# Optimization experiments

Measured on AMD Instinct MI355X. Metric: run time of the kernel, lower is better.

The kernel has to match this reference:

```python
import jax, jax.numpy as jnp
import numpy as np

DIM = 192
HEADS = 4
EPS_LN = 1e-5
EPS_NORM = 1e-12


def _layernorm(x, w, b):
    # x: [b, c, h, w]; normalize over channel dim (equiv to 'b (h w) c' LN over last axis)
    mu = jnp.mean(x, axis=1, keepdims=True)
    var = jnp.mean((x - mu) ** 2, axis=1, keepdims=True)
    return (x - mu) / jnp.sqrt(var + EPS_LN) * w[None, :, None, None] + b[None, :, None, None]


def _conv1x1(x, w):
    # w: [out_c, in_c]
    return jnp.einsum('bchw,oc->bohw', x, w)


def _dwconv3x3(x, w):
    # w: [c, 1, 3, 3], depthwise (groups = c), padding 1
    return jax.lax.conv_general_dilated(
        x, w, window_strides=(1, 1), padding='SAME',
        feature_group_count=x.shape[1],
        dimension_numbers=('NCHW', 'OIHW', 'NCHW'))


def _l2norm(x):
    # F.normalize(dim=-1): x / max(||x||_2, eps)
    n = jnp.sqrt(jnp.sum(x * x, axis=-1, keepdims=True))
    return x / jnp.maximum(n, EPS_NORM)


def setup_inputs() -> dict:
    key = jax.random.key(0)
    ks = jax.random.split(key, 10)
    b, c, h, w = 8, DIM, 128, 128
    inp = {
        'xx': jax.random.normal(ks[0], (b, c, h, w), jnp.float32),
        'q_in': jax.random.normal(ks[1], (b, c, h, w), jnp.float32),
        'ln_w': jnp.ones((c,), jnp.float32),
        'ln_b': jnp.zeros((c,), jnp.float32),
        'w_q': jax.random.normal(ks[2], (c, c), jnp.float32) * 0.02,
        'w_k': jax.random.normal(ks[3], (c, c), jnp.float32) * 0.02,
        'w_v': jax.random.normal(ks[4], (c, c), jnp.float32) * 0.02,
        'wd_q': jax.random.normal(ks[5], (c, 1, 3, 3), jnp.float32) * 0.1,
        'wd_k': jax.random.normal(ks[6], (c, 1, 3, 3), jnp.float32) * 0.1,
        'wd_v': jax.random.normal(ks[7], (c, 1, 3, 3), jnp.float32) * 0.1,
        'w_proj': jax.random.normal(ks[8], (c, c), jnp.float32) * 0.02,
        'temperature': jnp.ones((HEADS, 1, 1), jnp.float32),
    }
    return inp


def reference(xx, q_in, ln_w, ln_b, w_q, w_k, w_v, wd_q, wd_k, wd_v, w_proj, temperature):
    b, c, h, w = xx.shape
    hw = h * w
    dh = c // HEADS  # per-head channel dim

    x_n = _layernorm(xx, ln_w, ln_b)
    q_n = _layernorm(q_in, ln_w, ln_b)

    q = _dwconv3x3(_conv1x1(q_n, w_q), wd_q)
    k = _dwconv3x3(_conv1x1(x_n, w_k), wd_k)
    v = _dwconv3x3(_conv1x1(x_n, w_v), wd_v)

    # b (head c) h w -> b head c (h w)
    q = q.reshape(b, HEADS, dh, hw)
    k = k.reshape(b, HEADS, dh, hw)
    v = v.reshape(b, HEADS, dh, hw)

    q = _l2norm(q)
    k = _l2norm(k)

    # channel-channel attention: [b, head, dh, dh]
    attn = jnp.einsum('bhcn,bhdn->bhcd', q, k) * temperature[None]
    attn = jax.nn.softmax(attn, axis=-1)

    out = jnp.einsum('bhcd,bhdn->bhcn', attn, v)  # [b, head, dh, hw]
    out = out.reshape(b, c, h, w)
    out = _conv1x1(out, w_proj) + q_in
    return out
```

## Files before the change

kernel.cpp:

```cpp
#include <hip/hip_runtime.h>
#include <hip/hip_bf16.h>
#include <stdint.h>

#define HWSZ 16384
#define CCH 192
#define NB 8
#define NHEAD 4
#define DHEAD 48

typedef unsigned short u16;
typedef __bf16 bf16x8 __attribute__((ext_vector_type(8)));
typedef float f32x4 __attribute__((ext_vector_type(4)));
typedef short s16x8 __attribute__((ext_vector_type(8)));
typedef short s16x4 __attribute__((ext_vector_type(4)));

__device__ __forceinline__ float b2f(u16 h){
  union { unsigned u; float f; } v; v.u = ((unsigned)h) << 16; return v.f;
}
__device__ __forceinline__ u16 f2b(float f){
  union { float f; unsigned u; } v; v.f = f;
  unsigned r = v.u + 0x7fffu + ((v.u >> 16) & 1u);
  return (u16)(r >> 16);
}

__global__ __launch_bounds__(256) void k_wpack(
    const float* __restrict__ wq, const float* __restrict__ wk,
    const float* __restrict__ wv, u16* __restrict__ o)
{
  int m = blockIdx.x;
  const float* src = (m == 0) ? wq : (m == 1) ? wk : wv;
  u16* dst = o + (size_t)m * CCH * CCH;
  int tid = threadIdx.x;
  #pragma unroll
  for (int i = 0; i < 36; ++i){
    int e = (i * 256 + tid) * 4;
    float4 v = *(const float4*)(src + e);
    s16x4 pk;
    pk[0] = (short)f2b(v.x); pk[1] = (short)f2b(v.y);
    pk[2] = (short)f2b(v.z); pk[3] = (short)f2b(v.w);
    *(s16x4*)(dst + e) = pk;
  }
}

template<int NG>
__global__ __launch_bounds__(256) void k_lngemm(
    const float* __restrict__ x, const float* __restrict__ lnw,
    const float* __restrict__ lnb,
    const u16* __restrict__ W0, const u16* __restrict__ W1,
    u16* __restrict__ O0, u16* __restrict__ O1)
{
  __shared__ u16 lnT[12672];
  __shared__ float red[2048];
  __shared__ float mures[128];
  __shared__ float lwlb[384];
  int tid = threadIdx.x;
  int b   = blockIdx.y;
  int p0  = blockIdx.x * 64;
  int cq  = tid >> 4;
  int q   = tid & 15;

  float wl = 0.f, bl = 0.f;
  if (tid >= 64){
    int c = tid - 64;
    wl = lnw[c]; bl = lnb[c];
  }

  float4 v[12];
  {
    const float* xb = x + (size_t)b * CCH * HWSZ + p0;
    #pragma unroll
    for (int i = 0; i < 12; ++i)
      v[i] = *(const float4*)(xb + (size_t)(i * 16 + cq) * HWSZ + q * 4);
  }
  {
    float4 ps  = make_float4(0.f, 0.f, 0.f, 0.f);
    float4 pss = make_float4(0.f, 0.f, 0.f, 0.f);
    #pragma unroll
    for (int i = 0; i < 12; ++i){
      ps.x += v[i].x; ps.y += v[i].y; ps.z += v[i].z; ps.w += v[i].w;
      pss.x += v[i].x * v[i].x; pss.y += v[i].y * v[i].y;
      pss.z += v[i].z * v[i].z; pss.w += v[i].w * v[i].w;
    }
    *(float4*)(&red[cq * 64 + q * 4])        = ps;
    *(float4*)(&red[1024 + cq * 64 + q * 4]) = pss;
  }
  __syncthreads();

  if (tid < 64){
    float s = 0.f, ss2 = 0.f;
    #pragma unroll
    for (int j = 0; j < 16; ++j){
      s   += red[j * 64 + tid];
      ss2 += red[1024 + j * 64 + tid];
    }
    float mu  = s * (1.f / CCH);
    float var = ss2 * (1.f / CCH) - mu * mu;
    mures[tid]      = mu;
    mures[64 + tid] = rsqrtf(var + 1e-5f);
  } else {
    int c = tid - 64;
    lwlb[c] = wl; lwlb[192 + c] = bl;
  }
  __syncthreads();

  {
    float m0 = mures[q * 4 + 0], m1 = mures[q * 4 + 1];
    float m2 = mures[q * 4 + 2], m3 = mures[q * 4 + 3];
    float r0 = mures[64 + q * 4 + 0], r1 = mures[64 + q * 4 + 1];
    float r2 = mures[64 + q * 4 + 2], r3 = mures[64 + q * 4 + 3];
    #pragma unroll
    for (int i = 0; i < 12; ++i){
      int c = i * 16 + cq;
      float lw_ = lwlb[c], lb_ = lwlb[192 + c];
      s16x4 pk;
      pk[0] = (short)f2b((v[i].x - m0) * r0 * lw_ + lb_);
      pk[1] = (short)f2b((v[i].y - m1) * r1 * lw_ + lb_);
      pk[2] = (short)f2b((v[i].z - m2) * r2 * lw_ + lb_);
      pk[3] = (short)f2b((v[i].w - m3) * r3 * lw_ + lb_);
      int kb   = c >> 5, kr = c & 31;
      int tile = (kr >> 2) & 1;
      int mr   = ((kr >> 3) << 2) | (kr & 3);
      int ti   = (kb * 4 + (q >> 2)) * 2 + tile;
      *(s16x4*)(&lnT[ti * 264 + mr * 16 + (q & 3) * 4]) = pk;
    }
  }
  __syncthreads();

  int lane = tid & 63, wid = tid >> 6;
  int quad = lane >> 4, r = lane & 15;
  int wm = wid * 48;
  const u16* A0 = W0 + (size_t)wm * CCH;
  const u16* A1 = (NG == 2) ? (W1 + (size_t)wm * CCH) : nullptr;
  f32x4 acc0[3][4] = {};
  f32x4 acc1[3][4] = {};
  unsigned lvb = (unsigned)(uintptr_t)(&lnT[0]) + 2u * (unsigned)(r + quad * 64);
  #pragma unroll
  for (int kb = 0; kb < 6; ++kb){
    int k0 = kb * 32;
    bf16x8 a0[3], a1[3];
    #pragma unroll
    for (int i = 0; i < 3; ++i)
      a0[i] = *(const bf16x8*)(A0 + (size_t)(i * 16 + r) * CCH + k0 + quad * 8);
    if (NG == 2){
      #pragma unroll
      for (int i = 0; i < 3; ++i)
        a1[i] = *(const bf16x8*)(A1 + (size_t)(i * 16 + r) * CCH + k0 + quad * 8);
    }
    s16x4 lo[4], hi[4];
    #pragma unroll
    for (int j = 0; j < 4; ++j){
      unsigned a = lvb + (unsigned)kb * 4224u + (unsigned)j * 1056u;
      asm volatile("ds_read_b64_tr_b16 %0, %1" : "=&v"(lo[j]) : "v"(a));
      asm volatile("ds_read_b64_tr_b16 %0, %1 offset:528" : "=&v"(hi[j]) : "v"(a));
    }
    asm volatile("s_waitcnt lgkmcnt(0)" ::: "memory");
    __builtin_amdgcn_sched_barrier(0);
    #pragma unroll
    for (int j = 0; j < 4; ++j){
      union { s16x8 s; bf16x8 b; } u;
      u.s = __builtin_shufflevector(lo[j], hi[j], 0, 1, 2, 3, 4, 5, 6, 7);
      #pragma unroll
      for (int i = 0; i < 3; ++i)
        acc0[i][j] = __builtin_amdgcn_mfma_f32_16x16x32_bf16(a0[i], u.b, acc0[i][j], 0, 0, 0);
      if (NG == 2){
        #pragma unroll
        for (int i = 0; i < 3; ++i)
          acc1[i][j] = __builtin_amdgcn_mfma_f32_16x16x32_bf16(a1[i], u.b, acc1[i][j], 0, 0, 0);
      }
    }
  }
  size_t ob = (size_t)b * CCH * HWSZ;
  #pragma unroll
  for (int i = 0; i < 3; ++i){
    #pragma unroll
    for (int rg = 0; rg < 4; ++rg){
      int o = wm + i * 16 + quad * 4 + rg;
      size_t rowb = ob + (size_t)o * HWSZ;
      #pragma unroll
      for (int j = 0; j < 4; ++j){
        int n = p0 + j * 16 + r;
        O0[rowb + n] = f2b(acc0[i][j][rg]);
        if (NG == 2) O1[rowb + n] = f2b(acc1[i][j][rg]);
      }
    }
  }
}

__global__ __launch_bounds__(256) void k_dw3(
    const float* __restrict__ wq, const float* __restrict__ wk,
    const float* __restrict__ wv,
    u16* __restrict__ bq, u16* __restrict__ bk, u16* __restrict__ bv,
    float* __restrict__ ssq_q, float* __restrict__ ssq_k)
{
  int tid = threadIdx.x;
  int bc  = blockIdx.x;
  int z   = blockIdx.y;
  int c   = bc % CCH;
  const float* wd = (z == 0) ? wq : (z == 1) ? wk : wv;
  u16* buf = (z == 0) ? bq : (z == 1) ? bk : bv;
  float w[9];
  #pragma unroll
  for (int t = 0; t < 9; ++t) w[t] = wd[c * 9 + t];
  u16* p = buf + (size_t)bc * HWSZ;

  int xseg = tid & 15, ygrp = tid >> 4;
  int x0 = xseg * 8, y0 = ygrp * 8;

  s16x8 zz = {0,0,0,0,0,0,0,0};
  s16x8 raw[10];
  #pragma unroll
  for (int rr = 0; rr < 10; ++rr){
    int yy = y0 - 1 + rr;
    raw[rr] = (yy >= 0 && yy < 128) ? *(const s16x8*)(p + yy * 128 + x0) : zz;
  }
  __syncthreads();

  float cf[10][8];
  float lf[10], rgt[10];
  #pragma unroll
  for (int rr = 0; rr < 10; ++rr){
    #pragma unroll
    for (int j = 0; j < 8; ++j) cf[rr][j] = b2f((u16)raw[rr][j]);
    float l  = __shfl_up(cf[rr][7], 1);
    float rr_ = __shfl_down(cf[rr][0], 1);
    lf[rr]  = (xseg > 0)  ? l   : 0.f;
    rgt[rr] = (xseg < 15) ? rr_ : 0.f;
  }

  float ss = 0.f;
  #pragma unroll
  for (int k = 0; k < 8; ++k){
    float acc[8] = {0.f,0.f,0.f,0.f,0.f,0.f,0.f,0.f};
    #pragma unroll
    for (int dy = 0; dy < 3; ++dy){
      int rr = k + dy;
      float wl = w[dy * 3], wc = w[dy * 3 + 1], wr = w[dy * 3 + 2];
      acc[0] += wl * lf[rr] + wc * cf[rr][0] + wr * cf[rr][1];
      #pragma unroll
      for (int j = 1; j < 7; ++j)
        acc[j] += wl * cf[rr][j - 1] + wc * cf[rr][j] + wr * cf[rr][j + 1];
      acc[7] += wl * cf[rr][6] + wc * cf[rr][7] + wr * rgt[rr];
    }
    s16x8 pk;
    #pragma unroll
    for (int j = 0; j < 8; ++j){
      pk[j] = (short)f2b(acc[j]);
      ss += acc[j] * acc[j];
    }
    *(s16x8*)(p + (y0 + k) * 128 + x0) = pk;
  }

  if (z < 2){
    #pragma unroll
    for (int m = 32; m > 0; m >>= 1) ss += __shfl_xor(ss, m);
    if ((tid & 63) == 0) atomicAdd(&((z == 0) ? ssq_q : ssq_k)[bc], ss);
  }
}

__global__ void k_gram(const u16* __restrict__ q, const u16* __restrict__ k,
                       float* __restrict__ G)
{
  __shared__ float gs[4 * 48 * 49];
  int tid = threadIdx.x;
  int chunk = blockIdx.x;
  int h = blockIdx.y, b = blockIdx.z;
  int lane = tid & 63, w = tid >> 6;
  int quad = lane >> 4, r = lane & 15;
  int nb = chunk * 1024 + w * 256;
  const u16* qb = q + ((size_t)b * CCH + h * DHEAD) * HWSZ;
  const u16* kb = k + ((size_t)b * CCH + h * DHEAD) * HWSZ;
  f32x4 acc[3][3] = {};
  for (int s = 0; s < 8; ++s){
    int kk = nb + s * 32 + quad * 8;
    bf16x8 af[3], bfr[3];
    #pragma unroll
    for (int i = 0; i < 3; ++i){
      af[i]  = *(const bf16x8*)(qb + (size_t)(i * 16 + r) * HWSZ + kk);
      bfr[i] = *(const bf16x8*)(kb + (size_t)(i * 16 + r) * HWSZ + kk);
    }
    #pragma unroll
    for (int i = 0; i < 3; ++i)
      #pragma unroll
      for (int j = 0; j < 3; ++j)
        acc[i][j] = __builtin_amdgcn_mfma_f32_16x16x32_bf16(af[i], bfr[j], acc[i][j], 0, 0, 0);
  }
  float* gw = gs + w * (48 * 49);
  #pragma unroll
  for (int i = 0; i < 3; ++i)
    #pragma unroll
    for (int j = 0; j < 3; ++j)
      #pragma unroll
      for (int rg = 0; rg < 4; ++rg){
        int row = i * 16 + quad * 4 + rg;
        int col = j * 16 + r;
        gw[row * 49 + col] = acc[i][j][rg];
      }
  __syncthreads();
  float* gb = G + (size_t)(b * NHEAD + h) * (DHEAD * DHEAD);
  #pragma unroll
  for (int t = 0; t < 9; ++t){
    int e = t * 256 + tid;
    int row = e / 48, col = e - row * 48;
    int o = row * 49 + col;
    float s = gs[o] + gs[48 * 49 + o] + gs[2 * 48 * 49 + o] + gs[3 * 48 * 49 + o];
    atomicAdd(&gb[e], s);
  }
}

__global__ __launch_bounds__(256) void k_mk(
    const float* __restrict__ G, const float* __restrict__ ssq_q,
    const float* __restrict__ ssq_k, const float* __restrict__ temp,
    const float* __restrict__ wp, u16* __restrict__ Mout)
{
  __shared__ u16 Pt[48 * 72];
  __shared__ u16 wA[192 * 72];
  __shared__ float rks[48];
  int tid = threadIdx.x;
  int h = blockIdx.x, b = blockIdx.y;
  {
    s16x8 z = {};
    #pragma unroll
    for (int i = 0; i < 2; ++i){
      int idx = (i * 256 + tid) * 8;
      if (idx < 48 * 72) *(s16x8*)(&Pt[idx]) = z;
    }
    #pragma unroll
    for (int i = 0; i < 7; ++i){
      int idx = (i * 256 + tid) * 8;
      if (idx < 192 * 72) *(s16x8*)(&wA[idx]) = z;
    }
  }
  if (tid < DHEAD)
    rks[tid] = 1.f / fmaxf(sqrtf(ssq_k[b * CCH + h * DHEAD + tid]), 1e-12f);
  __syncthreads();
  if (tid < DHEAD){
    float rq = temp[h] / fmaxf(sqrtf(ssq_q[b * CCH + h * DHEAD + tid]), 1e-12f);
    const float* gr = G + (size_t)(b * NHEAD + h) * (DHEAD * DHEAD) + tid * DHEAD;
    float a[DHEAD];
    float mx = -1e30f;
    #pragma unroll
    for (int d = 0; d < DHEAD; ++d){
      a[d] = gr[d] * rq * rks[d];
      mx = fmaxf(mx, a[d]);
    }
    float sum = 0.f;
    #pragma unroll
    for (int d = 0; d < DHEAD; ++d){ a[d] = __expf(a[d] - mx); sum += a[d]; }
    float inv = 1.f / sum;
    #pragma unroll
    for (int d = 0; d < DHEAD; ++d) Pt[d * 72 + tid] = f2b(a[d] * inv);
  }
  {
    const float* wb = wp + h * DHEAD;
    #pragma unroll
    for (int i = 0; i < 9; ++i){
      int e = (i * 256 + tid) * 4;
      int row = e / DHEAD, col = e - row * DHEAD;
      float4 v = *(const float4*)(wb + (size_t)row * CCH + col);
      s16x4 pk;
      pk[0] = (short)f2b(v.x); pk[1] = (short)f2b(v.y);
      pk[2] = (short)f2b(v.z); pk[3] = (short)f2b(v.w);
      *(s16x4*)(&wA[row * 72 + col]) = pk;
    }
  }
  __syncthreads();
  int lane = tid & 63, wid = tid >> 6;
  int quad = lane >> 4, r = lane & 15;
  int wm = wid * 48;
  f32x4 acc[3][3] = {};
  #pragma unroll
  for (int ks = 0; ks < 2; ++ks){
    int k0 = ks * 32;
    bf16x8 af[3], bf[3];
    #pragma unroll
    for (int i = 0; i < 3; ++i)
      af[i] = *(const bf16x8*)(&wA[(wm + i * 16 + r) * 72 + k0 + quad * 8]);
    #pragma unroll
    for (int j = 0; j < 3; ++j)
      bf[j] = *(const bf16x8*)(&Pt[(j * 16 + r) * 72 + k0 + quad * 8]);
    #pragma unroll
    for (int i = 0; i < 3; ++i)
      #pragma unroll
      for (int j = 0; j < 3; ++j)
        acc[i][j] = __builtin_amdgcn_mfma_f32_16x16x32_bf16(af[i], bf[j], acc[i][j], 0, 0, 0);
  }
  u16* mb = Mout + (size_t)b * (CCH * CCH) + h * DHEAD;
  #pragma unroll
  for (int i = 0; i < 3; ++i)
    #pragma unroll
    for (int j = 0; j < 3; ++j)
      #pragma unroll
      for (int rg = 0; rg < 4; ++rg){
        int o = wm + i * 16 + quad * 4 + rg;
        int d = j * 16 + r;
        mb[(size_t)o * CCH + d] = f2b(acc[i][j][rg]);
      }
}

__global__ __launch_bounds__(256) void k_gemmv(
    const u16* __restrict__ M, const u16* __restrict__ V,
    float* __restrict__ Out, const float* __restrict__ resid)
{
  __shared__ u16 lA[64 * 200];
  __shared__ u16 lV[96 * 264];
  int tid = threadIdx.x;
  int n0 = blockIdx.x * 128;
  int m0 = blockIdx.y * 64;
  int b  = blockIdx.z;
  {
    const u16* ap = M + (size_t)b * (CCH * CCH) + m0 * CCH;
    #pragma unroll
    for (int i = 0; i < 6; ++i){
      int off = (i * 256 + tid) * 8;
      int row = off / CCH, col = off - row * CCH;
      *(int4*)(&lA[row * 200 + col]) = *(const int4*)(ap + off);
    }
  }
  {
    const u16* vp = V + (size_t)b * CCH * HWSZ + n0;
    #pragma unroll
    for (int i = 0; i < 12; ++i){
      int e = i * 256 + tid;
      int c = e >> 4, ns = (e & 15) * 8;
      int4 v = *(const int4*)(vp + (size_t)c * HWSZ + ns);
      int kb = c >> 5, kr = c & 31;
      int tile = (kr >> 2) & 1;
      int mr = ((kr >> 3) << 2) | (kr & 3);
      int ti = (kb * 8 + (ns >> 4)) * 2 + tile;
      *(int4*)(&lV[ti * 264 + mr * 16 + (ns & 15)]) = v;
    }
  }
  __syncthreads();
  int lane = tid & 63, wid = tid >> 6;
  int quad = lane >> 4, r = lane & 15;
  int wm = (wid >> 1) * 32, wn = (wid & 1) * 64;
  unsigned lvb = (unsigned)(uintptr_t)(&lV[0]) + 2u * (unsigned)(r + quad * 64)
               + (unsigned)((wn >> 4) * 2) * 528u;
  f32x4 acc[2][4] = {};
  #pragma unroll
  for (int kb = 0; kb < 6; ++kb){
    int k0 = kb * 32;
    s16x4 lo[4], hi[4];
    #pragma unroll
    for (int j = 0; j < 4; ++j){
      unsigned a = lvb + (unsigned)kb * 8448u + (unsigned)j * 1056u;
      asm volatile("ds_read_b64_tr_b16 %0, %1" : "=&v"(lo[j]) : "v"(a));
      asm volatile("ds_read_b64_tr_b16 %0, %1 offset:528" : "=&v"(hi[j]) : "v"(a));
    }
    bf16x8 af[2];
    #pragma unroll
    for (int i = 0; i < 2; ++i)
      af[i] = *(const bf16x8*)(&lA[(wm + i * 16 + r) * 200 + k0 + quad * 8]);
    asm volatile("s_waitcnt lgkmcnt(0)" ::: "memory");
    __builtin_amdgcn_sched_barrier(0);
    #pragma unroll
    for (int j = 0; j < 4; ++j){
      union { s16x8 s; bf16x8 b; } u;
      u.s = __builtin_shufflevector(lo[j], hi[j], 0, 1, 2, 3, 4, 5, 6, 7);
      #pragma unroll
      for (int i = 0; i < 2; ++i)
        acc[i][j] = __builtin_amdgcn_mfma_f32_16x16x32_bf16(af[i], u.b, acc[i][j], 0, 0, 0);
    }
  }
  size_t obase = (size_t)b * CCH * HWSZ;
  #pragma unroll
  for (int i = 0; i < 2; ++i){
    #pragma unroll
    for (int rg = 0; rg < 4; ++rg){
      int o = m0 + wm + i * 16 + quad * 4 + rg;
      size_t rowb = obase + (size_t)o * HWSZ;
      #pragma unroll
      for (int j = 0; j < 4; ++j){
        int n = n0 + wn + j * 16 + r;
        Out[rowb + n] = acc[i][j][rg] + resid[rowb + n];
      }
    }
  }
}

extern "C" void kernel_launch(void* const* d_in, const int* in_sizes, int n_in,
                              void* d_out, int out_size, void* d_ws, size_t ws_size,
                              hipStream_t stream)
{
  const float* xx     = (const float*)d_in[0];
  const float* q_in   = (const float*)d_in[1];
  const float* ln_w   = (const float*)d_in[2];
  const float* ln_b   = (const float*)d_in[3];
  const float* w_q    = (const float*)d_in[4];
  const float* w_k    = (const float*)d_in[5];
  const float* w_v    = (const float*)d_in[6];
  const float* wd_q   = (const float*)d_in[7];
  const float* wd_k   = (const float*)d_in[8];
  const float* wd_v   = (const float*)d_in[9];
  const float* w_proj = (const float*)d_in[10];
  const float* temp   = (const float*)d_in[11];

  const size_t SZ = (size_t)NB * CCH * HWSZ;
  u16* B1 = (u16*)d_ws;
  u16* B2 = B1 + SZ;
  u16* B3 = B2 + SZ;
  float* G     = (float*)(B3 + SZ);
  float* ssq_q = G + 32 * DHEAD * DHEAD;
  float* ssq_k = ssq_q + NB * CCH;
  u16* Mb      = (u16*)(ssq_k + NB * CCH);
  u16* Wb      = Mb + (size_t)NB * CCH * CCH;

  hipMemsetAsync(G, 0, (size_t)(32 * DHEAD * DHEAD + 2 * NB * CCH) * sizeof(float), stream);

  k_wpack<<<3, 256, 0, stream>>>(w_q, w_k, w_v, Wb);
  k_lngemm<2><<<dim3(256, NB), 256, 0, stream>>>(
      xx, ln_w, ln_b, Wb + CCH * CCH, Wb + 2 * CCH * CCH, B2, B1);
  k_lngemm<1><<<dim3(256, NB), 256, 0, stream>>>(
      q_in, ln_w, ln_b, Wb, nullptr, B3, nullptr);
  k_dw3<<<dim3(NB * CCH, 3), 256, 0, stream>>>(wd_q, wd_k, wd_v,
                                               B3, B2, B1, ssq_q, ssq_k);
  k_gram<<<dim3(16, NHEAD, NB), 256, 0, stream>>>(B3, B2, G);
  k_mk<<<dim3(NHEAD, NB), 256, 0, stream>>>(G, ssq_q, ssq_k, temp, w_proj, Mb);
  k_gemmv<<<dim3(128, 3, NB), 256, 0, stream>>>(Mb, B1, (float*)d_out, q_in);
}
```

Measured before the change: 437.6 us.

## Split LN+GEMM kernels into 512-thread blocks to cut register pressure

The templated LN+1x1-conv kernel becomes two 512-thread kernels. In the two-output version, each group of four waves computes one weight matrix, so each wave holds a single accumulator set. Input values are re-read from global memory after the statistics pass instead of staying in registers. The single-output version processes 128 pixels per block with two LDS tiles. The aim is lower register use and higher occupancy, at the cost of a second global read of the input tile and larger shared-memory use per block.

Measured after the change: 442.1 us. About the same (+1.0%).

```diff
diff --git a/kernel.cpp b/kernel.cpp
--- a/kernel.cpp
+++ b/kernel.cpp
@@ -42,15 +42,14 @@
   }
 }
 
-template<int NG>
-__global__ __launch_bounds__(256) void k_lngemm(
+__global__ __launch_bounds__(512, 4) void k_lngemm2(
     const float* __restrict__ x, const float* __restrict__ lnw,
     const float* __restrict__ lnb,
     const u16* __restrict__ W0, const u16* __restrict__ W1,
     u16* __restrict__ O0, u16* __restrict__ O1)
 {
   __shared__ u16 lnT[12672];
-  __shared__ float red[2048];
+  __shared__ float red[4096];
   __shared__ float mures[128];
   __shared__ float lwlb[384];
   int tid = threadIdx.x;
@@ -59,19 +58,137 @@
   int cq  = tid >> 4;
   int q   = tid & 15;
 
-  float wl = 0.f, bl = 0.f;
-  if (tid >= 64){
-    int c = tid - 64;
-    wl = lnw[c]; bl = lnb[c];
-  }
+  if (tid >= 128 && tid < 320)      lwlb[tid - 128]       = lnw[tid - 128];
+  else if (tid >= 320)              lwlb[192 + tid - 320] = lnb[tid - 320];
+
+  const float* xb = x + (size_t)b * CCH * HWSZ + p0;
+
+  {
+    float4 t[6];
+    #pragma unroll
+    for (int i = 0; i < 6; ++i)
+      t[i] = *(const float4*)(xb + (size_t)(i * 32 + cq) * HWSZ + q * 4);
+    float4 ps  = make_float4(0.f, 0.f, 0.f, 0.f);
+    float4 pss = make_float4(0.f, 0.f, 0.f, 0.f);
+    #pragma unroll
+    for (int i = 0; i < 6; ++i){
+      ps.x += t[i].x; ps.y += t[i].y; ps.z += t[i].z; ps.w += t[i].w;
+      pss.x += t[i].x * t[i].x; pss.y += t[i].y * t[i].y;
+      pss.z += t[i].z * t[i].z; pss.w += t[i].w * t[i].w;
+    }
+    *(float4*)(&red[cq * 64 + q * 4])        = ps;
+    *(float4*)(&red[2048 + cq * 64 + q * 4]) = pss;
+  }
+  __syncthreads();
+
+  if (tid < 64){
+    float s = 0.f, ss2 = 0.f;
+    #pragma unroll
+    for (int j = 0; j < 32; ++j){
+      s   += red[j * 64 + tid];
+      ss2 += red[2048 + j * 64 + tid];
+    }
+    float mu  = s * (1.f / CCH);
+    float var = ss2 * (1.f / CCH) - mu * mu;
+    mures[tid]      = mu;
+    mures[64 + tid] = rsqrtf(var + 1e-5f);
+  }
+  __syncthreads();
+
+  {
+    const float* xb2 = xb;
+    { uint64_t pp = (uint64_t)xb2; asm volatile("" : "+s"(pp)); xb2 = (const float*)pp; }
+    float4 m4 = *(const float4*)(&mures[q * 4]);
+    float4 r4 = *(const float4*)(&mures[64 + q * 4]);
+    #pragma unroll
+    for (int i = 0; i < 6; ++i){
+      int c = i * 32 + cq;
+      float4 v = *(const float4*)(xb2 + (size_t)c * HWSZ + q * 4);
+      float lw_ = lwlb[c], lb_ = lwlb[192 + c];
+      s16x4 pk;
+      pk[0] = (short)f2b((v.x - m4.x) * r4.x * lw_ + lb_);
+      pk[1] = (short)f2b((v.y - m4.y) * r4.y * lw_ + lb_);
+      pk[2] = (short)f2b((v.z - m4.z) * r4.z * lw_ + lb_);
+      pk[3] = (short)f2b((v.w - m4.w) * r4.w * lw_ + lb_);
+      int kr   = cq;
+      int tile = (kr >> 2) & 1;
+      int mr   = ((kr >> 3) << 2) | (kr & 3);
+      int ti   = (i * 4 + (q >> 2)) * 2 + tile;
+      *(s16x4*)(&lnT[ti * 264 + mr * 16 + (q & 3) * 4]) = pk;
+    }
+  }
+  __syncthreads();
+
+  int lane = tid & 63, wid = tid >> 6;
+  int quad = lane >> 4, r = lane & 15;
+  int mat = wid >> 2, w4 = wid & 3;
+  int wm = w4 * 48;
+  const u16* A0 = (mat ? W1 : W0) + (size_t)wm * CCH;
+  f32x4 acc[3][4] = {};
+  unsigned lvb = (unsigned)(uintptr_t)(&lnT[0]) + 2u * (unsigned)(r + quad * 64);
+  #pragma unroll
+  for (int kb = 0; kb < 6; ++kb){
+    int k0 = kb * 32;
+    bf16x8 a0[3];
+    #pragma unroll
+    for (int i = 0; i < 3; ++i)
+      a0[i] = *(const bf16x8*)(A0 + (size_t)(i * 16 + r) * CCH + k0 + quad * 8);
+    s16x4 lo[4], hi[4];
+    #pragma unroll
+    for (int j = 0; j < 4; ++j){
+      unsigned a = lvb + (unsigned)kb * 4224u + (unsigned)j * 1056u;
+      asm volatile("ds_read_b64_tr_b16 %0, %1" : "=&v"(lo[j]) : "v"(a));
+      asm volatile("ds_read_b64_tr_b16 %0, %1 offset:528" : "=&v"(hi[j]) : "v"(a));
+    }
+    asm volatile("s_waitcnt lgkmcnt(0)" ::: "memory");
+    __builtin_amdgcn_sched_barrier(0);
+    #pragma unroll
+    for (int j = 0; j < 4; ++j){
+      union { s16x8 s; bf16x8 b; } u;
+      u.s = __builtin_shufflevector(lo[j], hi[j], 0, 1, 2, 3, 4, 5, 6, 7);
+      #pragma unroll
+      for (int i = 0; i < 3; ++i)
+        acc[i][j] = __builtin_amdgcn_mfma_f32_16x16x32_bf16(a0[i], u.b, acc[i][j], 0, 0, 0);
+    }
+  }
+  u16* O = mat ? O1 : O0;
+  size_t ob = (size_t)b * CCH * HWSZ;
+  #pragma unroll
+  for (int i = 0; i < 3; ++i){
+    #pragma unroll
+    for (int rg = 0; rg < 4; ++rg){
+      int o = wm + i * 16 + quad * 4 + rg;
+      size_t rowb = ob + (size_t)o * HWSZ;
+      #pragma unroll
+      for (int j = 0; j < 4; ++j)
+        O[rowb + p0 + j * 16 + r] = f2b(acc[i][j][rg]);
+    }
+  }
+}
+
+__global__ __launch_bounds__(512, 4) void k_lngemm1(
+    const float* __restrict__ x, const float* __restrict__ lnw,
+    const float* __restrict__ lnb,
+    const u16* __restrict__ W0, u16* __restrict__ O0)
+{
+  __shared__ u16 lnT[2][12672];
+  __shared__ float red[4096];
+  __shared__ float mures[256];
+  __shared__ float lwlb[384];
+  int tid = threadIdx.x;
+  int b   = blockIdx.y;
+  int p0  = blockIdx.x * 128;
+  int cg  = tid >> 5;
+  int q32 = tid & 31;
+
+  if (tid >= 128 && tid < 320)      lwlb[tid - 128]       = lnw[tid - 128];
+  else if (tid >= 320)              lwlb[192 + tid - 320] = lnb[tid - 320];
 
   float4 v[12];
-  {
-    const float* xb = x + (size_t)b * CCH * HWSZ + p0;
-    #pragma unroll
-    for (int i = 0; i < 12; ++i)
-      v[i] = *(const float4*)(xb + (size_t)(i * 16 + cq) * HWSZ + q * 4);
-  }
+  const float* xb = x + (size_t)b * CCH * HWSZ + p0;
+  #pragma unroll
+  for (int i = 0; i < 12; ++i)
+    v[i] = *(const float4*)(xb + (size_t)(i * 16 + cg) * HWSZ + q32 * 4);
   {
     float4 ps  = make_float4(0.f, 0.f, 0.f, 0.f);
     float4 pss = make_float4(0.f, 0.f, 0.f, 0.f);
@@ -81,71 +198,61 @@
       pss.x += v[i].x * v[i].x; pss.y += v[i].y * v[i].y;
       pss.z += v[i].z * v[i].z; pss.w += v[i].w * v[i].w;
     }
-    *(float4*)(&red[cq * 64 + q * 4])        = ps;
-    *(float4*)(&red[1024 + cq * 64 + q * 4]) = pss;
-  }
-  __syncthreads();
-
-  if (tid < 64){
+    *(float4*)(&red[cg * 128 + q32 * 4])        = ps;
+    *(float4*)(&red[2048 + cg * 128 + q32 * 4]) = pss;
+  }
+  __syncthreads();
+
+  if (tid < 128){
     float s = 0.f, ss2 = 0.f;
     #pragma unroll
     for (int j = 0; j < 16; ++j){
-      s   += red[j * 64 + tid];
-      ss2 += red[1024 + j * 64 + tid];
+      s   += red[j * 128 + tid];
+      ss2 += red[2048 + j * 128 + tid];
     }
     float mu  = s * (1.f / CCH);
     float var = ss2 * (1.f / CCH) - mu * mu;
-    mures[tid]      = mu;
-    mures[64 + tid] = rsqrtf(var + 1e-5f);
-  } else {
-    int c = tid - 64;
-    lwlb[c] = wl; lwlb[192 + c] = bl;
-  }
-  __syncthreads();
-
-  {
-    float m0 = mures[q * 4 + 0], m1 = mures[q * 4 + 1];
-    float m2 = mures[q * 4 + 2], m3 = mures[q * 4 + 3];
-    float r0 = mures[64 + q * 4 + 0], r1 = mures[64 + q * 4 + 1];
-    float r2 = mures[64 + q * 4 + 2], r3 = mures[64 + q * 4 + 3];
+    mures[tid]       = mu;
+    mures[128 + tid] = rsqrtf(var + 1e-5f);
+  }
+  __syncthreads();
+
+  {
+    float4 m4 = *(const float4*)(&mures[q32 * 4]);
+    float4 r4 = *(const float4*)(&mures[128 + q32 * 4]);
+    int sub = q32 >> 4, q = q32 & 15;
     #pragma unroll
     for (int i = 0; i < 12; ++i){
-      int c = i * 16 + cq;
+      int c = i * 16 + cg;
       float lw_ = lwlb[c], lb_ = lwlb[192 + c];
       s16x4 pk;
-      pk[0] = (short)f2b((v[i].x - m0) * r0 * lw_ + lb_);
-      pk[1] = (short)f2b((v[i].y - m1) * r1 * lw_ + lb_);
-      pk[2] = (short)f2b((v[i].z - m2) * r2 * lw_ + lb_);
-      pk[3] = (short)f2b((v[i].w - m3) * r3 * lw_ + lb_);
+      pk[0] = (short)f2b((v[i].x - m4.x) * r4.x * lw_ + lb_);
+      pk[1] = (short)f2b((v[i].y - m4.y) * r4.y * lw_ + lb_);
+      pk[2] = (short)f2b((v[i].z - m4.z) * r4.z * lw_ + lb_);
+      pk[3] = (short)f2b((v[i].w - m4.w) * r4.w * lw_ + lb_);
       int kb   = c >> 5, kr = c & 31;
       int tile = (kr >> 2) & 1;
       int mr   = ((kr >> 3) << 2) | (kr & 3);
       int ti   = (kb * 4 + (q >> 2)) * 2 + tile;
-      *(s16x4*)(&lnT[ti * 264 + mr * 16 + (q & 3) * 4]) = pk;
+      *(s16x4*)(&lnT[sub][ti * 264 + mr * 16 + (q & 3) * 4]) = pk;
     }
   }
   __syncthreads();
 
   int lane = tid & 63, wid = tid >> 6;
   int quad = lane >> 4, r = lane & 15;
-  int wm = wid * 48;
+  int sub = wid >> 2, w4 = wid & 3;
+  int wm = w4 * 48;
   const u16* A0 = W0 + (size_t)wm * CCH;
-  const u16* A1 = (NG == 2) ? (W1 + (size_t)wm * CCH) : nullptr;
-  f32x4 acc0[3][4] = {};
-  f32x4 acc1[3][4] = {};
-  unsigned lvb = (unsigned)(uintptr_t)(&lnT[0]) + 2u * (unsigned)(r + quad * 64);
+  f32x4 acc[3][4] = {};
+  unsigned lvb = (unsigned)(uintptr_t)(&lnT[sub][0]) + 2u * (unsigned)(r + quad * 64);
   #pragma unroll
   for (int kb = 0; kb < 6; ++kb){
     int k0 = kb * 32;
-    bf16x8 a0[3], a1[3];
+    bf16x8 a0[3];
     #pragma unroll
     for (int i = 0; i < 3; ++i)
       a0[i] = *(const bf16x8*)(A0 + (size_t)(i * 16 + r) * CCH + k0 + quad * 8);
-    if (NG == 2){
-      #pragma unroll
-      for (int i = 0; i < 3; ++i)
-        a1[i] = *(const bf16x8*)(A1 + (size_t)(i * 16 + r) * CCH + k0 + quad * 8);
-    }
     s16x4 lo[4], hi[4];
     #pragma unroll
     for (int j = 0; j < 4; ++j){
@@ -161,12 +268,7 @@
       u.s = __builtin_shufflevector(lo[j], hi[j], 0, 1, 2, 3, 4, 5, 6, 7);
       #pragma unroll
       for (int i = 0; i < 3; ++i)
-        acc0[i][j] = __builtin_amdgcn_mfma_f32_16x16x32_bf16(a0[i], u.b, acc0[i][j], 0, 0, 0);
-      if (NG == 2){
-        #pragma unroll
-        for (int i = 0; i < 3; ++i)
-          acc1[i][j] = __builtin_amdgcn_mfma_f32_16x16x32_bf16(a1[i], u.b, acc1[i][j], 0, 0, 0);
-      }
+        acc[i][j] = __builtin_amdgcn_mfma_f32_16x16x32_bf16(a0[i], u.b, acc[i][j], 0, 0, 0);
     }
   }
   size_t ob = (size_t)b * CCH * HWSZ;
@@ -177,11 +279,8 @@
       int o = wm + i * 16 + quad * 4 + rg;
       size_t rowb = ob + (size_t)o * HWSZ;
       #pragma unroll
-      for (int j = 0; j < 4; ++j){
-        int n = p0 + j * 16 + r;
-        O0[rowb + n] = f2b(acc0[i][j][rg]);
-        if (NG == 2) O1[rowb + n] = f2b(acc1[i][j][rg]);
-      }
+      for (int j = 0; j < 4; ++j)
+        O0[rowb + p0 + sub * 64 + j * 16 + r] = f2b(acc[i][j][rg]);
     }
   }
 }
@@ -508,10 +607,10 @@
   hipMemsetAsync(G, 0, (size_t)(32 * DHEAD * DHEAD + 2 * NB * CCH) * sizeof(float), stream);
 
   k_wpack<<<3, 256, 0, stream>>>(w_q, w_k, w_v, Wb);
-  k_lngemm<2><<<dim3(256, NB), 256, 0, stream>>>(
+  k_lngemm2<<<dim3(256, NB), 512, 0, stream>>>(
       xx, ln_w, ln_b, Wb + CCH * CCH, Wb + 2 * CCH * CCH, B2, B1);
-  k_lngemm<1><<<dim3(256, NB), 256, 0, stream>>>(
-      q_in, ln_w, ln_b, Wb, nullptr, B3, nullptr);
+  k_lngemm1<<<dim3(128, NB), 512, 0, stream>>>(
+      q_in, ln_w, ln_b, Wb, B3);
   k_dw3<<<dim3(NB * CCH, 3), 256, 0, stream>>>(wd_q, wd_k, wd_v,
                                                B3, B2, B1, ssq_q, ssq_k);
   k_gram<<<dim3(16, NHEAD, NB), 256, 0, stream>>>(B3, B2, G);
```

## Split LayerNorm stats into separate pass and merge both 1x1 conv GEMMs

Applied to the files above, without the earlier changes.

Computes per-pixel LayerNorm mean and inverse std in a separate streaming kernel, then one merged 512-thread kernel handles both inputs (z selects xx or q_in). It normalizes a 128-pixel tile and runs the K/V or Q GEMMs across 8 waves, with weight fragments prefetched one k-block ahead. The goal is more parallelism per block and fewer launches, with the reduction taken out of the GEMM kernel. The cost is reading both inputs an extra time for the stats pass plus a stats buffer round trip through memory.

Result: slower. 476.0 us (+8.8%).

```diff
diff --git a/kernel.cpp b/kernel.cpp
--- a/kernel.cpp
+++ b/kernel.cpp
@@ -42,145 +42,136 @@
   }
 }
 
-template<int NG>
-__global__ __launch_bounds__(256) void k_lngemm(
-    const float* __restrict__ x, const float* __restrict__ lnw,
-    const float* __restrict__ lnb,
-    const u16* __restrict__ W0, const u16* __restrict__ W1,
-    u16* __restrict__ O0, u16* __restrict__ O1)
-{
-  __shared__ u16 lnT[12672];
-  __shared__ float red[2048];
-  __shared__ float mures[128];
-  __shared__ float lwlb[384];
+__global__ __launch_bounds__(256) void k_stats(
+    const float* __restrict__ xx, const float* __restrict__ q_in,
+    float* __restrict__ st)
+{
+  int tid = threadIdx.x;
+  int px  = blockIdx.x * 256 + tid;
+  int b   = blockIdx.y, sel = blockIdx.z;
+  const float* in = (sel ? q_in : xx) + (size_t)b * CCH * HWSZ + px;
+  float s0 = 0.f, s1 = 0.f, q0 = 0.f, q1 = 0.f;
+  #pragma unroll 8
+  for (int c = 0; c < CCH; c += 2){
+    float va = in[(size_t)c * HWSZ];
+    float vb = in[(size_t)(c + 1) * HWSZ];
+    s0 += va; q0 += va * va;
+    s1 += vb; q1 += vb * vb;
+  }
+  float s = s0 + s1, ss = q0 + q1;
+  float mu  = s * (1.f / CCH);
+  float var = ss * (1.f / CCH) - mu * mu;
+  float2 o = make_float2(mu, rsqrtf(var + 1e-5f));
+  *(float2*)(st + ((size_t)(sel * NB + b) * HWSZ + px) * 2) = o;
+}
+
+__global__ __launch_bounds__(512) void k_conv(
+    const float* __restrict__ xx, const float* __restrict__ q_in,
+    const float* __restrict__ St,
+    const float* __restrict__ lnw, const float* __restrict__ lnb,
+    const u16* __restrict__ Wb,
+    u16* __restrict__ Ok, u16* __restrict__ Ov, u16* __restrict__ Oq)
+{
+  __shared__ u16 lnT[96 * 264];
   int tid = threadIdx.x;
   int b   = blockIdx.y;
-  int p0  = blockIdx.x * 64;
-  int cq  = tid >> 4;
-  int q   = tid & 15;
-
-  float wl = 0.f, bl = 0.f;
-  if (tid >= 64){
-    int c = tid - 64;
-    wl = lnw[c]; bl = lnb[c];
-  }
-
-  float4 v[12];
+  int z   = blockIdx.z;
+  int p0  = blockIdx.x * 128;
+
   {
-    const float* xb = x + (size_t)b * CCH * HWSZ + p0;
-    #pragma unroll
-    for (int i = 0; i < 12; ++i)
-      v[i] = *(const float4*)(xb + (size_t)(i * 16 + cq) * HWSZ + q * 4);
-  }
-  {
-    float4 ps  = make_float4(0.f, 0.f, 0.f, 0.f);
-    float4 pss = make_float4(0.f, 0.f, 0.f, 0.f);
-    #pragma unroll
-    for (int i = 0; i < 12; ++i){
-      ps.x += v[i].x; ps.y += v[i].y; ps.z += v[i].z; ps.w += v[i].w;
-      pss.x += v[i].x * v[i].x; pss.y += v[i].y * v[i].y;
-      pss.z += v[i].z * v[i].z; pss.w += v[i].w * v[i].w;
-    }
-    *(float4*)(&red[cq * 64 + q * 4])        = ps;
-    *(float4*)(&red[1024 + cq * 64 + q * 4]) = pss;
-  }
-  __syncthreads();
-
-  if (tid < 64){
-    float s = 0.f, ss2 = 0.f;
-    #pragma unroll
-    for (int j = 0; j < 16; ++j){
-      s   += red[j * 64 + tid];
-      ss2 += red[1024 + j * 64 + tid];
-    }
-    float mu  = s * (1.f / CCH);
-    float var = ss2 * (1.f / CCH) - mu * mu;
-    mures[tid]      = mu;
-    mures[64 + tid] = rsqrtf(var + 1e-5f);
-  } else {
-    int c = tid - 64;
-    lwlb[c] = wl; lwlb[192 + c] = bl;
-  }
-  __syncthreads();
-
-  {
-    float m0 = mures[q * 4 + 0], m1 = mures[q * 4 + 1];
-    float m2 = mures[q * 4 + 2], m3 = mures[q * 4 + 3];
-    float r0 = mures[64 + q * 4 + 0], r1 = mures[64 + q * 4 + 1];
-    float r2 = mures[64 + q * 4 + 2], r3 = mures[64 + q * 4 + 3];
-    #pragma unroll
-    for (int i = 0; i < 12; ++i){
-      int c = i * 16 + cq;
-      float lw_ = lwlb[c], lb_ = lwlb[192 + c];
-      s16x4 pk;
-      pk[0] = (short)f2b((v[i].x - m0) * r0 * lw_ + lb_);
-      pk[1] = (short)f2b((v[i].y - m1) * r1 * lw_ + lb_);
-      pk[2] = (short)f2b((v[i].z - m2) * r2 * lw_ + lb_);
-      pk[3] = (short)f2b((v[i].w - m3) * r3 * lw_ + lb_);
+    const float* xb = (z ? q_in : xx) + (size_t)b * CCH * HWSZ + p0;
+    const float* sb = St + ((size_t)(z * NB + b) * HWSZ + p0) * 2;
+    #pragma unroll
+    for (int i = 0; i < 6; ++i){
+      int e = i * 512 + tid;
+      int c = e >> 4, ns = (e & 15) * 8;
+      float4 v0 = *(const float4*)(xb + (size_t)c * HWSZ + ns);
+      float4 v1 = *(const float4*)(xb + (size_t)c * HWSZ + ns + 4);
+      float4 t0 = *(const float4*)(sb + ns * 2);
+      float4 t1 = *(const float4*)(sb + ns * 2 + 4);
+      float4 t2 = *(const float4*)(sb + ns * 2 + 8);
+      float4 t3 = *(const float4*)(sb + ns * 2 + 12);
+      float lw_ = lnw[c], lb_ = lnb[c];
+      s16x8 pk;
+      pk[0] = (short)f2b((v0.x - t0.x) * t0.y * lw_ + lb_);
+      pk[1] = (short)f2b((v0.y - t0.z) * t0.w * lw_ + lb_);
+      pk[2] = (short)f2b((v0.z - t1.x) * t1.y * lw_ + lb_);
+      pk[3] = (short)f2b((v0.w - t1.z) * t1.w * lw_ + lb_);
+      pk[4] = (short)f2b((v1.x - t2.x) * t2.y * lw_ + lb_);
+      pk[5] = (short)f2b((v1.y - t2.z) * t2.w * lw_ + lb_);
+      pk[6] = (short)f2b((v1.z - t3.x) * t3.y * lw_ + lb_);
+      pk[7] = (short)f2b((v1.w - t3.z) * t3.w * lw_ + lb_);
       int kb   = c >> 5, kr = c & 31;
       int tile = (kr >> 2) & 1;
       int mr   = ((kr >> 3) << 2) | (kr & 3);
-      int ti   = (kb * 4 + (q >> 2)) * 2 + tile;
-      *(s16x4*)(&lnT[ti * 264 + mr * 16 + (q & 3) * 4]) = pk;
+      int ti   = (kb * 8 + (ns >> 4)) * 2 + tile;
+      *(s16x8*)(&lnT[ti * 264 + mr * 16 + (ns & 15)]) = pk;
     }
   }
   __syncthreads();
 
   int lane = tid & 63, wid = tid >> 6;
   int quad = lane >> 4, r = lane & 15;
-  int wm = wid * 48;
-  const u16* A0 = W0 + (size_t)wm * CCH;
-  const u16* A1 = (NG == 2) ? (W1 + (size_t)wm * CCH) : nullptr;
-  f32x4 acc0[3][4] = {};
-  f32x4 acc1[3][4] = {};
-  unsigned lvb = (unsigned)(uintptr_t)(&lnT[0]) + 2u * (unsigned)(r + quad * 64);
-  #pragma unroll
-  for (int kb = 0; kb < 6; ++kb){
-    int k0 = kb * 32;
-    bf16x8 a0[3], a1[3];
+  int mq = wid & 3;
+  int wm = mq * 48;
+  const u16* W;
+  u16* O;
+  if (z == 0){
+    W = Wb + (size_t)((wid >> 2) + 1) * CCH * CCH;
+    O = (wid >> 2) ? Ov : Ok;
+  } else {
+    W = Wb;
+    O = Oq;
+  }
+  int nt  = z ? 1 : 2;
+  int nhS = z ? (wid >> 2) : 0;
+  const u16* A0 = W + (size_t)wm * CCH;
+  unsigned lvb0 = (unsigned)(uintptr_t)(&lnT[0]) + 2u * (unsigned)(r + quad * 64);
+  size_t ob = (size_t)b * CCH * HWSZ;
+
+  for (int t = 0; t < nt; ++t){
+    int nh = z ? nhS : t;
+    f32x4 acc[3][4] = {};
+    bf16x8 aC[3], aN[3];
     #pragma unroll
     for (int i = 0; i < 3; ++i)
-      a0[i] = *(const bf16x8*)(A0 + (size_t)(i * 16 + r) * CCH + k0 + quad * 8);
-    if (NG == 2){
-      #pragma unroll
-      for (int i = 0; i < 3; ++i)
-        a1[i] = *(const bf16x8*)(A1 + (size_t)(i * 16 + r) * CCH + k0 + quad * 8);
-    }
-    s16x4 lo[4], hi[4];
-    #pragma unroll
-    for (int j = 0; j < 4; ++j){
-      unsigned a = lvb + (unsigned)kb * 4224u + (unsigned)j * 1056u;
-      asm volatile("ds_read_b64_tr_b16 %0, %1" : "=&v"(lo[j]) : "v"(a));
-      asm volatile("ds_read_b64_tr_b16 %0, %1 offset:528" : "=&v"(hi[j]) : "v"(a));
-    }
-    asm volatile("s_waitcnt lgkmcnt(0)" ::: "memory");
-    __builtin_amdgcn_sched_barrier(0);
-    #pragma unroll
-    for (int j = 0; j < 4; ++j){
-      union { s16x8 s; bf16x8 b; } u;
-      u.s = __builtin_shufflevector(lo[j], hi[j], 0, 1, 2, 3, 4, 5, 6, 7);
-      #pragma unroll
-      for (int i = 0; i < 3; ++i)
-        acc0[i][j] = __builtin_amdgcn_mfma_f32_16x16x32_bf16(a0[i], u.b, acc0[i][j], 0, 0, 0);
-      if (NG == 2){
+      aC[i] = *(const bf16x8*)(A0 + (size_t)(i * 16 + r) * CCH + quad * 8);
+    #pragma unroll
+    for (int kb = 0; kb < 6; ++kb){
+      s16x4 lo[4], hi[4];
+      #pragma unroll
+      for (int j = 0; j < 4; ++j){
+        unsigned a = lvb0 + (unsigned)(kb * 8448 + (nh * 4 + j) * 1056);
+        asm volatile("ds_read_b64_tr_b16 %0, %1" : "=&v"(lo[j]) : "v"(a));
+        asm volatile("ds_read_b64_tr_b16 %0, %1 offset:528" : "=&v"(hi[j]) : "v"(a));
+      }
+      if (kb < 5){
         #pragma unroll
         for (int i = 0; i < 3; ++i)
-          acc1[i][j] = __builtin_amdgcn_mfma_f32_16x16x32_bf16(a1[i], u.b, acc1[i][j], 0, 0, 0);
-      }
-    }
-  }
-  size_t ob = (size_t)b * CCH * HWSZ;
-  #pragma unroll
-  for (int i = 0; i < 3; ++i){
-    #pragma unroll
-    for (int rg = 0; rg < 4; ++rg){
-      int o = wm + i * 16 + quad * 4 + rg;
-      size_t rowb = ob + (size_t)o * HWSZ;
+          aN[i] = *(const bf16x8*)(A0 + (size_t)(i * 16 + r) * CCH + (kb + 1) * 32 + quad * 8);
+      }
+      asm volatile("s_waitcnt lgkmcnt(0)" ::: "memory");
+      __builtin_amdgcn_sched_barrier(0);
       #pragma unroll
       for (int j = 0; j < 4; ++j){
-        int n = p0 + j * 16 + r;
-        O0[rowb + n] = f2b(acc0[i][j][rg]);
-        if (NG == 2) O1[rowb + n] = f2b(acc1[i][j][rg]);
+        union { s16x8 s; bf16x8 b; } u;
+        u.s = __builtin_shufflevector(lo[j], hi[j], 0, 1, 2, 3, 4, 5, 6, 7);
+        #pragma unroll
+        for (int i = 0; i < 3; ++i)
+          acc[i][j] = __builtin_amdgcn_mfma_f32_16x16x32_bf16(aC[i], u.b, acc[i][j], 0, 0, 0);
+      }
+      #pragma unroll
+      for (int i = 0; i < 3; ++i) aC[i] = aN[i];
+    }
+    #pragma unroll
+    for (int i = 0; i < 3; ++i){
+      #pragma unroll
+      for (int rg = 0; rg < 4; ++rg){
+        int o = wm + i * 16 + quad * 4 + rg;
+        size_t rowb = ob + (size_t)o * HWSZ;
+        #pragma unroll
+        for (int j = 0; j < 4; ++j)
+          O[rowb + p0 + nh * 64 + j * 16 + r] = f2b(acc[i][j][rg]);
       }
     }
   }
@@ -504,14 +495,14 @@
   float* ssq_k = ssq_q + NB * CCH;
   u16* Mb      = (u16*)(ssq_k + NB * CCH);
   u16* Wb      = Mb + (size_t)NB * CCH * CCH;
+  float* Sb    = (float*)(Wb + 3 * CCH * CCH);
 
   hipMemsetAsync(G, 0, (size_t)(32 * DHEAD * DHEAD + 2 * NB * CCH) * sizeof(float), stream);
 
+  k_stats<<<dim3(64, NB, 2), 256, 0, stream>>>(xx, q_in, Sb);
   k_wpack<<<3, 256, 0, stream>>>(w_q, w_k, w_v, Wb);
-  k_lngemm<2><<<dim3(256, NB), 256, 0, stream>>>(
-      xx, ln_w, ln_b, Wb + CCH * CCH, Wb + 2 * CCH * CCH, B2, B1);
-  k_lngemm<1><<<dim3(256, NB), 256, 0, stream>>>(
-      q_in, ln_w, ln_b, Wb, nullptr, B3, nullptr);
+  k_conv<<<dim3(128, NB, 2), 512, 0, stream>>>(
+      xx, q_in, Sb, ln_w, ln_b, Wb, B2, B1, B3);
   k_dw3<<<dim3(NB * CCH, 3), 256, 0, stream>>>(wd_q, wd_k, wd_v,
                                                B3, B2, B1, ssq_q, ssq_k);
   k_gram<<<dim3(16, NHEAD, NB), 256, 0, stream>>>(B3, B2, G);
```
